# Kernel tuning notes

Hardware: AMD Instinct MI355X
Metric: run time of the kernel (lower is better)

The kernel has to match this reference:

```python
import jax, jax.numpy as jnp
import numpy as np

D_MODEL = 1024
H = 16
DH = 64
FFN = 4096
CHUNK = 64
LN_EPS = 1e-5


def layer_norm(x, w, b):
    mu = x.mean(-1, keepdims=True)
    var = x.var(-1, keepdims=True)
    return (x - mu) * jax.lax.rsqrt(var + LN_EPS) * w + b


def l2_normalize(x):
    # matches torch F.normalize(p=2, dim=-1, eps=1e-12)
    n = jnp.sqrt(jnp.sum(x * x, axis=-1, keepdims=True))
    return x / jnp.maximum(n, 1e-12)


def chunk_gla(q, k, v, alpha, C=CHUNK):
    B, Hh, N, D = q.shape
    nc = N // C  # N chosen as multiple of C (pad==0 in original)
    q = q.reshape(B, Hh, nc, C, D)
    k = k.reshape(B, Hh, nc, C, D)
    v = v.reshape(B, Hh, nc, C, D)
    alpha = alpha.reshape(B, Hh, nc, C, D)

    log_a = jnp.log(jnp.maximum(alpha, 1e-6))
    la_cum = jnp.cumsum(log_a, axis=3)                  # (B,H,nc,C,D)
    la_mean = la_cum.mean(-1)                            # (B,H,nc,C)
    tril = jnp.tril(jnp.ones((C, C), dtype=q.dtype))
    decay = jnp.exp(la_mean[..., :, None] - la_mean[..., None, :]) * tril  # (B,H,nc,C,C)

    attn_intra = jnp.einsum('bhncd,bhnmd->bhncm', q, k) * decay
    o_intra = jnp.einsum('bhncm,bhnmd->bhncd', attn_intra, v)

    decay_to_end = jnp.exp(la_cum[:, :, :, -1:, :] - la_cum)
    kv_chunk = jnp.einsum('bhncf,bhnce->bhnfe', k * decay_to_end, v)  # (B,H,nc,D,D)
    chunk_decay = jnp.exp(log_a.sum(3))                  # (B,H,nc,D)
    q_dec = q * jnp.exp(la_cum)                          # decay_from_start

    def step(S, inp):
        qd, kv, cd = inp                                 # (B,H,C,D),(B,H,D,D),(B,H,D)
        o = jnp.einsum('bhcd,bhde->bhce', qd, S)
        S_new = S * cd[:, :, :, None] + kv
        return S_new, o

    S0 = jnp.zeros((B, Hh, D, D), dtype=q.dtype)
    _, o_inter = jax.lax.scan(
        step, S0,
        (jnp.moveaxis(q_dec, 2, 0), jnp.moveaxis(kv_chunk, 2, 0), jnp.moveaxis(chunk_decay, 2, 0)))
    o_inter = jnp.moveaxis(o_inter, 0, 2)                # (B,H,nc,C,D)
    return (o_intra + o_inter).reshape(B, Hh, N, D)


def setup_inputs() -> dict:
    key = jax.random.key(0)
    ks = jax.random.split(key, 16)
    s = 0.02
    td = H * DH
    return {
        'x': jax.random.normal(ks[0], (2, 4096, D_MODEL), dtype=jnp.float32),
        'Wq': jax.random.normal(ks[1], (D_MODEL, td), dtype=jnp.float32) * s,
        'Wk': jax.random.normal(ks[2], (D_MODEL, td), dtype=jnp.float32) * s,
        'Wv': jax.random.normal(ks[3], (D_MODEL, td), dtype=jnp.float32) * s,
        'Wg': jax.random.normal(ks[4], (D_MODEL, td), dtype=jnp.float32) * s,
        'bg': jnp.full((td,), -0.5, dtype=jnp.float32),
        'Wo': jax.random.normal(ks[5], (td, D_MODEL), dtype=jnp.float32) * s,
        'ln1_w': jnp.ones((D_MODEL,), jnp.float32),
        'ln1_b': jnp.zeros((D_MODEL,), jnp.float32),
        'ln2_w': jnp.ones((D_MODEL,), jnp.float32),
        'ln2_b': jnp.zeros((D_MODEL,), jnp.float32),
        'W1': jax.random.normal(ks[6], (D_MODEL, FFN), dtype=jnp.float32) * s,
        'b1': jnp.zeros((FFN,), jnp.float32),
        'W2': jax.random.normal(ks[7], (FFN, D_MODEL), dtype=jnp.float32) * s,
        'b2': jnp.zeros((D_MODEL,), jnp.float32),
    }


def reference(x, Wq, Wk, Wv, Wg, bg, Wo, ln1_w, ln1_b, ln2_w, ln2_b, W1, b1, W2, b2):
    B, N, _ = x.shape
    xn = layer_norm(x, ln1_w, ln1_b)
    q = (xn @ Wq).reshape(B, N, H, DH).transpose(0, 2, 1, 3)
    k = (xn @ Wk).reshape(B, N, H, DH).transpose(0, 2, 1, 3)
    v = (xn @ Wv).reshape(B, N, H, DH).transpose(0, 2, 1, 3)
    q = l2_normalize(q)
    k = l2_normalize(k)
    alpha = jax.nn.sigmoid(xn @ Wg + bg).reshape(B, N, H, DH).transpose(0, 2, 1, 3)
    o = chunk_gla(q, k, v, alpha)
    o = o.transpose(0, 2, 1, 3).reshape(B, N, H * DH)
    x = x + o @ Wo  # dropout off (eval / p=0)
    h = layer_norm(x, ln2_w, ln2_b)
    x = x + jax.nn.gelu(h @ W1 + b1, approximate=False) @ W2 + b2
    return x
```

## Files before the change

kernel.cpp:

```cpp
#include <hip/hip_runtime.h>

#define AS1 __attribute__((address_space(1)))
#define AS3 __attribute__((address_space(3)))

typedef unsigned short u16;
typedef short s16x8 __attribute__((ext_vector_type(8)));
typedef float f32x4 __attribute__((ext_vector_type(4)));
typedef float f32x16 __attribute__((ext_vector_type(16)));

__device__ __forceinline__ float bf2f(u16 u) {
    union { unsigned u; float f; } v; v.u = ((unsigned)u) << 16; return v.f;
}
__device__ __forceinline__ u16 f2bf(float f) {
    union { float f; unsigned u; } v; v.f = f;
    unsigned u = v.u;
    return (u16)((u + 0x7FFFu + ((u >> 16) & 1u)) >> 16);
}

__device__ __forceinline__ void gload16(const void* g, void* l) {
    __builtin_amdgcn_global_load_lds((const AS1 void*)g, (AS3 void*)l, 16, 0, 0);
}

__global__ __launch_bounds__(256) void transpose_bf16(
    const float* __restrict__ src, u16* __restrict__ dst, int R, int C)
{
    __shared__ float t[32][33];
    const int tx = threadIdx.x, ty = threadIdx.y;
    const int r0 = blockIdx.x * 32, c0 = blockIdx.y * 32;
#pragma unroll
    for (int i = 0; i < 4; i++)
        t[ty + i * 8][tx] = src[(size_t)(r0 + ty + i * 8) * C + c0 + tx];
    __syncthreads();
#pragma unroll
    for (int i = 0; i < 4; i++)
        dst[(size_t)(c0 + ty + i * 8) * R + r0 + tx] = f2bf(t[tx][ty + i * 8]);
}

__global__ __launch_bounds__(256) void ln_bf16(
    const float* __restrict__ x, const float* __restrict__ w,
    const float* __restrict__ b, u16* __restrict__ out)
{
    __shared__ float red[8];
    const int row = blockIdx.x;
    const int tid = threadIdx.x;
    const size_t base = (size_t)row * 1024 + tid * 4;
    const float4 xv = *(const float4*)&x[base];
    float s = xv.x + xv.y + xv.z + xv.w;
    float q = xv.x * xv.x + xv.y * xv.y + xv.z * xv.z + xv.w * xv.w;
#pragma unroll
    for (int m = 1; m < 64; m <<= 1) { s += __shfl_xor(s, m); q += __shfl_xor(q, m); }
    if ((tid & 63) == 0) { red[tid >> 6] = s; red[4 + (tid >> 6)] = q; }
    __syncthreads();
    s = red[0] + red[1] + red[2] + red[3];
    q = red[4] + red[5] + red[6] + red[7];
    const float mu = s * (1.f / 1024.f);
    const float var = q * (1.f / 1024.f) - mu * mu;
    const float rs = rsqrtf(var + 1e-5f);
    const float4 wv = *(const float4*)&w[tid * 4];
    const float4 bv = *(const float4*)&b[tid * 4];
    uint2 ov;
    ov.x = (unsigned)f2bf((xv.x - mu) * rs * wv.x + bv.x) |
           ((unsigned)f2bf((xv.y - mu) * rs * wv.y + bv.y) << 16);
    ov.y = (unsigned)f2bf((xv.z - mu) * rs * wv.z + bv.z) |
           ((unsigned)f2bf((xv.w - mu) * rs * wv.w + bv.w) << 16);
    *(uint2*)&out[base] = ov;
}

template <int EPX>
__global__ __launch_bounds__(256, 3) void gemmS(
    const u16* __restrict__ A, const u16* __restrict__ BT,
    float* __restrict__ Cf, u16* __restrict__ Cb,
    const float* __restrict__ bias, const float* __restrict__ resid,
    int M, int N, int K)
{
    __shared__ u16 As[8192];
    __shared__ u16 Bs[8192];
    const int tid = threadIdx.x;
    const int w = tid >> 6, l = tid & 63;

    const int gx = gridDim.x;
    const int nb = gx * gridDim.y;
    const int bid0 = blockIdx.y * gx + blockIdx.x;
    const int swz = (bid0 & 7) * (nb >> 3) + (bid0 >> 3);
    const int tm = (swz % gx) * 128;
    const int tn = (swz / gx) * 128;

    const int wm = (w >> 1) * 64, wn = (w & 1) * 64;

    const int srow = l >> 3;
    const int sg = ((l & 7) ^ srow) * 8;
    size_t aSb[4], bSb[4];
#pragma unroll
    for (int j = 0; j < 4; j++) {
        aSb[j] = (size_t)(tm + j * 32 + w * 8 + srow) * K + sg;
        bSb[j] = (size_t)(tn + j * 32 + w * 8 + srow) * K + sg;
    }

    const int la = l & 31, hi = l >> 5, key = l & 7;
    int aoff[2][4], boff[2][4];
#pragma unroll
    for (int mm = 0; mm < 2; mm++)
#pragma unroll
        for (int ks = 0; ks < 4; ks++) {
            const int g = ((ks * 2 + hi) ^ key) * 8;
            aoff[mm][ks] = (wm + mm * 32 + la) * 64 + g;
            boff[mm][ks] = (wn + mm * 32 + la) * 64 + g;
        }

    f32x16 acc[2][2] = {};

#pragma unroll
    for (int j = 0; j < 4; j++) {
        gload16(&A[aSb[j]], &As[(j * 32 + w * 8) * 64]);
        gload16(&BT[bSb[j]], &Bs[(j * 32 + w * 8) * 64]);
    }

    const int NT = K >> 6;
    for (int t = 0; t < NT; ++t) {
        __syncthreads();
#pragma unroll
        for (int ks = 0; ks < 4; ks++) {
            s16x8 a0 = *(const s16x8*)&As[aoff[0][ks]];
            s16x8 a1 = *(const s16x8*)&As[aoff[1][ks]];
            s16x8 b0 = *(const s16x8*)&Bs[boff[0][ks]];
            s16x8 b1 = *(const s16x8*)&Bs[boff[1][ks]];
            acc[0][0] = __builtin_amdgcn_mfma_f32_32x32x16_bf16(a0, b0, acc[0][0], 0, 0, 0);
            acc[0][1] = __builtin_amdgcn_mfma_f32_32x32x16_bf16(a0, b1, acc[0][1], 0, 0, 0);
            acc[1][0] = __builtin_amdgcn_mfma_f32_32x32x16_bf16(a1, b0, acc[1][0], 0, 0, 0);
            acc[1][1] = __builtin_amdgcn_mfma_f32_32x32x16_bf16(a1, b1, acc[1][1], 0, 0, 0);
        }
        if (t + 1 < NT) {
            __syncthreads();
            const int k0 = (t + 1) * 64;
#pragma unroll
            for (int j = 0; j < 4; j++) {
                gload16(&A[aSb[j] + k0], &As[(j * 32 + w * 8) * 64]);
                gload16(&BT[bSb[j] + k0], &Bs[(j * 32 + w * 8) * 64]);
            }
        }
    }

#pragma unroll
    for (int mm = 0; mm < 2; mm++)
#pragma unroll
        for (int nn = 0; nn < 2; nn++)
#pragma unroll
            for (int reg = 0; reg < 16; reg++) {
                const int row = tm + wm + mm * 32 + hi * 4 + (reg & 3) + (reg >> 2) * 8;
                const int col = tn + wn + nn * 32 + la;
                const float v = acc[mm][nn][reg];
                if (EPX == 0) {
                    if (col < 3072) Cb[(size_t)row * 3072 + col] = f2bf(v);
                    else            Cf[(size_t)row * 1024 + (col - 3072)] = v;
                } else if (EPX == 1) {
                    const float u2 = v + bias[col];
                    Cb[(size_t)row * N + col] =
                        f2bf(0.5f * u2 * (1.f + erff(u2 * 0.70710678118654752f)));
                } else if (EPX == 2) {
                    const size_t idx = (size_t)row * N + col;
                    Cf[idx] = v + resid[idx];
                } else {
                    const size_t idx = (size_t)row * N + col;
                    Cf[idx] = v + bias[col] + resid[idx];
                }
            }
}

#define TP 72
#define LP 65
__global__ __launch_bounds__(256) void gla_a(
    const u16* __restrict__ qkv,
    const float* __restrict__ g,
    const float* __restrict__ bg,
    u16* __restrict__ qdec,
    u16* __restrict__ kvT,
    float* __restrict__ cdec,
    u16* __restrict__ ointra)
{
    __shared__ u16 Qh[64 * TP];
    __shared__ u16 Kh[64 * TP];
    __shared__ u16 VT[64 * TP];
    __shared__ float L[64 * LP];
    __shared__ float lm[64], nq[64], nk[64];

    const int bid = blockIdx.x;
    const int bh = bid >> 6, ck = bid & 63;
    const int b = bh >> 4, h = bh & 15;
    const int tok0 = b * 4096 + ck * 64;
    const int tid = threadIdx.x;
    const int w = tid >> 6, l = tid & 63;

#pragma unroll
    for (int pass = 0; pass < 2; pass++) {
        const int c = (tid >> 3) + pass * 32;
        const int col = (tid & 7) * 8;
        const size_t rb = (size_t)(tok0 + c) * 3072 + h * 64 + col;
        uint4 qv = *(const uint4*)&qkv[rb];
        uint4 kv_ = *(const uint4*)&qkv[rb + 1024];
        uint4 vv = *(const uint4*)&qkv[rb + 2048];
        *(uint4*)&Qh[c * TP + col] = qv;
        *(uint4*)&Kh[c * TP + col] = kv_;
        const u16* va = (const u16*)&vv;
#pragma unroll
        for (int j = 0; j < 8; j++) VT[(col + j) * TP + c] = va[j];
    }
#pragma unroll
    for (int pass = 0; pass < 4; pass++) {
        const int c = (tid >> 4) + pass * 16;
        const int col = (tid & 15) * 4;
        float4 gv = *(const float4*)&g[(size_t)(tok0 + c) * 1024 + h * 64 + col];
        float4 bgv = *(const float4*)&bg[h * 64 + col];
        const float* ga = (const float*)&gv;
        const float* ba = (const float*)&bgv;
#pragma unroll
        for (int i = 0; i < 4; i++) {
            const float z = ga[i] + ba[i];
            const float al = 1.f / (1.f + __expf(-z));
            L[c * LP + col + i] = __logf(fmaxf(al, 1e-6f));
        }
    }
    __syncthreads();

    {
        const int d = tid >> 2, qq = tid & 3;
        float vals[16];
#pragma unroll
        for (int i = 0; i < 16; i++) vals[i] = L[(qq * 16 + i) * LP + d];
        float s = 0.f;
#pragma unroll
        for (int i = 0; i < 16; i++) { s += vals[i]; vals[i] = s; }
        float sum = s;
        float u1 = __shfl_up(sum, 1, 4); if (qq >= 1) sum += u1;
        float u2 = __shfl_up(sum, 2, 4); if (qq >= 2) sum += u2;
        const float excl = sum - s;
#pragma unroll
        for (int i = 0; i < 16; i++) L[(qq * 16 + i) * LP + d] = vals[i] + excl;
        if (qq == 3) cdec[((size_t)bh * 64 + ck) * 64 + d] = __expf(sum);
    }
    __syncthreads();

    {
        const int c = tid >> 2, qq = tid & 3;
        float sl = 0.f, sq = 0.f, sk = 0.f;
        uint4 qa = *(const uint4*)&Qh[c * TP + qq * 16];
        uint4 qb = *(const uint4*)&Qh[c * TP + qq * 16 + 8];
        uint4 ka = *(const uint4*)&Kh[c * TP + qq * 16];
        uint4 kb = *(const uint4*)&Kh[c * TP + qq * 16 + 8];
        const u16* qu = (const u16*)&qa; const u16* qu2 = (const u16*)&qb;
        const u16* ku = (const u16*)&ka; const u16* ku2 = (const u16*)&kb;
#pragma unroll
        for (int i = 0; i < 8; i++) {
            float q1 = bf2f(qu[i]), q2 = bf2f(qu2[i]);
            float k1 = bf2f(ku[i]), k2 = bf2f(ku2[i]);
            sq += q1 * q1 + q2 * q2;
            sk += k1 * k1 + k2 * k2;
        }
#pragma unroll
        for (int i = 0; i < 16; i++) sl += L[c * LP + qq * 16 + i];
        sl += __shfl_xor(sl, 1); sl += __shfl_xor(sl, 2);
        sq += __shfl_xor(sq, 1); sq += __shfl_xor(sq, 2);
        sk += __shfl_xor(sk, 1); sk += __shfl_xor(sk, 2);
        if (qq == 0) {
            lm[c] = sl * (1.f / 64.f);
            nq[c] = 1.f / fmaxf(sqrtf(sq), 1e-12f);
            nk[c] = 1.f / fmaxf(sqrtf(sk), 1e-12f);
        }
    }
    __syncthreads();

    u16 kdt[16];
    {
        const int c = tid >> 2, qq = tid & 3;
        const float qn = nq[c], kn = nk[c];
        uint4 qa = *(const uint4*)&Qh[c * TP + qq * 16];
        uint4 qb = *(const uint4*)&Qh[c * TP + qq * 16 + 8];
        uint4 ka = *(const uint4*)&Kh[c * TP + qq * 16];
        uint4 kb = *(const uint4*)&Kh[c * TP + qq * 16 + 8];
        u16* qu = (u16*)&qa; u16* qu2 = (u16*)&qb;
        u16* ku = (u16*)&ka; u16* ku2 = (u16*)&kb;
        float Lc[16], Le[16];
#pragma unroll
        for (int i = 0; i < 16; i++) {
            Lc[i] = L[c * LP + qq * 16 + i];
            Le[i] = L[63 * LP + qq * 16 + i];
        }
        unsigned pk[8];
#pragma unroll
        for (int i = 0; i < 8; i++) {
            float qh1 = bf2f(qu[i]) * qn;  qu[i] = f2bf(qh1);
            float qh2 = bf2f(qu2[i]) * qn; qu2[i] = f2bf(qh2);
            float kh1 = bf2f(ku[i]) * kn;  ku[i] = f2bf(kh1);
            float kh2 = bf2f(ku2[i]) * kn; ku2[i] = f2bf(kh2);
            kdt[i]     = f2bf(kh1 * __expf(Le[i] - Lc[i]));
            kdt[i + 8] = f2bf(kh2 * __expf(Le[i + 8] - Lc[i + 8]));
        }
#pragma unroll
        for (int i = 0; i < 4; i++) {
            pk[i] = (unsigned)f2bf(bf2f(qu[2 * i]) * __expf(Lc[2 * i])) |
                    ((unsigned)f2bf(bf2f(qu[2 * i + 1]) * __expf(Lc[2 * i + 1])) << 16);
            pk[4 + i] = (unsigned)f2bf(bf2f(qu2[2 * i]) * __expf(Lc[8 + 2 * i])) |
                        ((unsigned)f2bf(bf2f(qu2[2 * i + 1]) * __expf(Lc[8 + 2 * i + 1])) << 16);
        }
        *(uint4*)&Qh[c * TP + qq * 16] = qa;
        *(uint4*)&Qh[c * TP + qq * 16 + 8] = qb;
        *(uint4*)&Kh[c * TP + qq * 16] = ka;
        *(uint4*)&Kh[c * TP + qq * 16 + 8] = kb;
        u16* qrow = &qdec[((size_t)bh * 4096 + ck * 64 + c) * 64 + qq * 16];
        *(uint4*)&qrow[0] = *(const uint4*)&pk[0];
        *(uint4*)&qrow[8] = *(const uint4*)&pk[4];
    }
    __syncthreads();

    u16* KDT = (u16*)L;
    {
        const int c = tid >> 2, qq = tid & 3;
#pragma unroll
        for (int i = 0; i < 16; i++) KDT[(qq * 16 + i) * TP + c] = kdt[i];
    }
    const int fr = l & 15;
    const int kk = (l >> 4) * 8;
    f32x4 accS[4] = {};
#pragma unroll
    for (int ks = 0; ks < 2; ks++) {
        s16x8 af = *(const s16x8*)&Qh[(w * 16 + fr) * TP + ks * 32 + kk];
#pragma unroll
        for (int j = 0; j < 4; j++) {
            s16x8 bf = *(const s16x8*)&Kh[(j * 16 + fr) * TP + ks * 32 + kk];
            accS[j] = __builtin_amdgcn_mfma_f32_16x16x32_bf16(af, bf, accS[j], 0, 0, 0);
        }
    }
    __syncthreads();

    {
        const int erow = w * 16 + (l >> 4) * 4;
#pragma unroll
        for (int j = 0; j < 4; j++) {
            const int mm = j * 16 + (l & 15);
            const float lmm = lm[mm];
#pragma unroll
            for (int r = 0; r < 4; r++) {
                const int cc = erow + r;
                const float wgt = (mm <= cc) ? __expf(lm[cc] - lmm) : 0.f;
                Qh[cc * TP + mm] = f2bf(accS[j][r] * wgt);
            }
        }
    }
    __syncthreads();

    f32x4 accO[4] = {};
    f32x4 accK[4] = {};
#pragma unroll
    for (int ks = 0; ks < 2; ks++) {
        s16x8 aAt = *(const s16x8*)&Qh[(w * 16 + fr) * TP + ks * 32 + kk];
        s16x8 aVt = *(const s16x8*)&VT[(w * 16 + fr) * TP + ks * 32 + kk];
#pragma unroll
        for (int j = 0; j < 4; j++) {
            s16x8 bVt = *(const s16x8*)&VT[(j * 16 + fr) * TP + ks * 32 + kk];
            s16x8 bKd = *(const s16x8*)&KDT[(j * 16 + fr) * TP + ks * 32 + kk];
            accO[j] = __builtin_amdgcn_mfma_f32_16x16x32_bf16(aAt, bVt, accO[j], 0, 0, 0);
            accK[j] = __builtin_amdgcn_mfma_f32_16x16x32_bf16(aVt, bKd, accK[j], 0, 0, 0);
        }
    }
    {
        const int erow = w * 16 + (l >> 4) * 4;
#pragma unroll
        for (int j = 0; j < 4; j++) {
            const int col = j * 16 + (l & 15);
#pragma unroll
            for (int r = 0; r < 4; r++) {
                const int row = erow + r;
                ointra[((size_t)bh * 4096 + ck * 64 + row) * 64 + col] = f2bf(accO[j][r]);
                kvT[(((size_t)bh * 64 + ck) * 64 + row) * 64 + col] = f2bf(accK[j][r]);
            }
        }
    }
}

__global__ __launch_bounds__(256) void gla_scan(
    const u16* __restrict__ kvT, const float* __restrict__ cdec,
    u16* __restrict__ ST)
{
    const int bh = blockIdx.x >> 4;
    const int de = (blockIdx.x & 15) * 256 + threadIdx.x;
    const int d = de & 63;
    float s = 0.f;
    const size_t base = (size_t)bh * 64 * 4096 + de;
    const size_t cb = (size_t)bh * 4096 + d;
    for (int t = 0; t < 64; t++) {
        ST[base + (size_t)t * 4096] = f2bf(s);
        s = s * cdec[cb + (size_t)t * 64] + bf2f(kvT[base + (size_t)t * 4096]);
    }
}

__global__ __launch_bounds__(256) void gla_b(
    const u16* __restrict__ qdec, const u16* __restrict__ ST,
    const u16* __restrict__ ointra, u16* __restrict__ obf)
{
    __shared__ u16 Qd[64 * TP];
    __shared__ u16 Sd[64 * TP];
    const int bid = blockIdx.x;
    const int bh = bid >> 6, ck = bid & 63;
    const int b = bh >> 4, h = bh & 15;
    const int tid = threadIdx.x;
    const int w = tid >> 6, l = tid & 63;
#pragma unroll
    for (int pass = 0; pass < 2; pass++) {
        const int r = (tid >> 3) + pass * 32;
        const int col = (tid & 7) * 8;
        *(uint4*)&Qd[r * TP + col] =
            *(const uint4*)&qdec[((size_t)bh * 4096 + ck * 64 + r) * 64 + col];
        *(uint4*)&Sd[r * TP + col] =
            *(const uint4*)&ST[(((size_t)bh * 64 + ck) * 64 + r) * 64 + col];
    }
    __syncthreads();
    const int fr = l & 15;
    const int kk = (l >> 4) * 8;
    f32x4 acc[4] = {};
#pragma unroll
    for (int ks = 0; ks < 2; ks++) {
        s16x8 af = *(const s16x8*)&Qd[(w * 16 + fr) * TP + ks * 32 + kk];
#pragma unroll
        for (int j = 0; j < 4; j++) {
            s16x8 bf = *(const s16x8*)&Sd[(j * 16 + fr) * TP + ks * 32 + kk];
            acc[j] = __builtin_amdgcn_mfma_f32_16x16x32_bf16(af, bf, acc[j], 0, 0, 0);
        }
    }
    const int erow = w * 16 + (l >> 4) * 4;
#pragma unroll
    for (int j = 0; j < 4; j++) {
        const int e = j * 16 + (l & 15);
#pragma unroll
        for (int r = 0; r < 4; r++) {
            const int cc = erow + r;
            const size_t ia = ((size_t)bh * 4096 + ck * 64 + cc) * 64 + e;
            const float v = acc[j][r] + bf2f(ointra[ia]);
            obf[(size_t)(b * 4096 + ck * 64 + cc) * 1024 + h * 64 + e] = f2bf(v);
        }
    }
}

__global__ void fill_sentinel(float* out, int n) {
    int i = blockIdx.x * 256 + threadIdx.x;
    if (i < n) out[i] = 12345.0f;
}

extern "C" void kernel_launch(void* const* d_in, const int* in_sizes, int n_in,
                              void* d_out, int out_size, void* d_ws, size_t ws_size,
                              hipStream_t stream)
{
    const float* x    = (const float*)d_in[0];
    const float* Wq   = (const float*)d_in[1];
    const float* Wk   = (const float*)d_in[2];
    const float* Wv   = (const float*)d_in[3];
    const float* Wg   = (const float*)d_in[4];
    const float* bg   = (const float*)d_in[5];
    const float* Wo   = (const float*)d_in[6];
    const float* ln1w = (const float*)d_in[7];
    const float* ln1b = (const float*)d_in[8];
    const float* ln2w = (const float*)d_in[9];
    const float* ln2b = (const float*)d_in[10];
    const float* W1   = (const float*)d_in[11];
    const float* b1   = (const float*)d_in[12];
    const float* W2   = (const float*)d_in[13];
    const float* b2   = (const float*)d_in[14];
    float* out = (float*)d_out;

    char* ws = (char*)d_ws;
    u16*   wtQKVG = (u16*)(ws + 0);
    u16*   wtWo   = (u16*)(ws + 8388608);
    u16*   wtW1   = (u16*)(ws + 10485760);
    u16*   wtW2   = (u16*)(ws + 18874368);
    u16*   xnb    = (u16*)(ws + 27262976);
    u16*   qkvb   = (u16*)(ws + 44040192);
    float* gbuf   = (float*)(ws + 94371840);
    u16*   kvT    = (u16*)(ws + 127926272);
    float* cdbuf  = (float*)(ws + 144703488);
    u16*   qdecb  = (u16*)(ws + 145227776);
    u16*   ointra = (u16*)(ws + 162004992);
    u16*   STb    = (u16*)(ws + 178782208);
    u16*   obf    = (u16*)(ws + 195559424);
    u16*   hbf    = (u16*)(ws + 212336640);
    float* x2     = (float*)(ws + 94371840);
    u16*   ffnb   = (u16*)(ws + 27262976);

    if (ws_size < 229113856u) {
        fill_sentinel<<<dim3((out_size + 255) / 256), dim3(256), 0, stream>>>(out, out_size);
        return;
    }

    const dim3 b256(256), b32x8(32, 8);

    transpose_bf16<<<dim3(32, 32),  b32x8, 0, stream>>>(Wq, wtQKVG,               1024, 1024);
    transpose_bf16<<<dim3(32, 32),  b32x8, 0, stream>>>(Wk, wtQKVG + 1024 * 1024, 1024, 1024);
    transpose_bf16<<<dim3(32, 32),  b32x8, 0, stream>>>(Wv, wtQKVG + 2048 * 1024, 1024, 1024);
    transpose_bf16<<<dim3(32, 32),  b32x8, 0, stream>>>(Wg, wtQKVG + 3072 * 1024, 1024, 1024);
    transpose_bf16<<<dim3(32, 32),  b32x8, 0, stream>>>(Wo, wtWo,                 1024, 1024);
    transpose_bf16<<<dim3(32, 128), b32x8, 0, stream>>>(W1, wtW1,                 1024, 4096);
    transpose_bf16<<<dim3(128, 32), b32x8, 0, stream>>>(W2, wtW2,                 4096, 1024);

    ln_bf16<<<dim3(8192), b256, 0, stream>>>(x, ln1w, ln1b, xnb);
    gemmS<0><<<dim3(64, 32), b256, 0, stream>>>(xnb, wtQKVG, gbuf, qkvb, nullptr, nullptr, 8192, 4096, 1024);

    gla_a<<<dim3(2048), b256, 0, stream>>>(qkvb, gbuf, bg, qdecb, kvT, cdbuf, ointra);
    gla_scan<<<dim3(512), b256, 0, stream>>>(kvT, cdbuf, STb);
    gla_b<<<dim3(2048), b256, 0, stream>>>(qdecb, STb, ointra, obf);

    gemmS<2><<<dim3(64, 8), b256, 0, stream>>>(obf, wtWo, x2, nullptr, nullptr, x, 8192, 1024, 1024);
    ln_bf16<<<dim3(8192), b256, 0, stream>>>(x2, ln2w, ln2b, hbf);
    gemmS<1><<<dim3(64, 32), b256, 0, stream>>>(hbf, wtW1, nullptr, ffnb, b1, nullptr, 8192, 4096, 1024);
    gemmS<4><<<dim3(64, 8), b256, 0, stream>>>(ffnb, wtW2, out, nullptr, b2, x2, 8192, 1024, 4096);
}
```

Before: 454.3 us.

## Add 256x128 tile GEMM for wide QKVG and FFN1 projections

Introduces a new gemmW kernel with a 256x128 output tile (each wave computing 128x64), used for the two N=4096 GEMMs (QKVG projection and FFN up with GELU). The goal is more reuse of the B tile per block and fewer LDS loads per MFMA. The cost is more LDS, a larger accumulator register footprint and occupancy dropping to 2 blocks. It also removes the block-index swizzle from gemmS, which may hurt L2 locality for the remaining N=1024 GEMMs.

```diff
diff --git a/kernel.cpp b/kernel.cpp
--- a/kernel.cpp
+++ b/kernel.cpp
@@ -67,9 +67,96 @@
 }
 
 template <int EPX>
+__global__ __launch_bounds__(256, 2) void gemmW(
+    const u16* __restrict__ A, const u16* __restrict__ BT,
+    float* __restrict__ Cf, u16* __restrict__ Cb,
+    const float* __restrict__ bias, int M, int N, int K)
+{
+    __shared__ u16 As[256 * 64];
+    __shared__ u16 Bs[128 * 64];
+    const int tid = threadIdx.x;
+    const int w = tid >> 6, l = tid & 63;
+    const int tm = blockIdx.x * 256, tn = blockIdx.y * 128;
+    const int wr = w >> 1, wc = w & 1;
+
+    const int srow = l >> 3;
+    const int sg = ((l & 7) ^ srow) * 8;
+    size_t aSb[8], bSb[4];
+#pragma unroll
+    for (int j = 0; j < 8; j++)
+        aSb[j] = (size_t)(tm + w * 64 + j * 8 + srow) * K + sg;
+#pragma unroll
+    for (int j = 0; j < 4; j++)
+        bSb[j] = (size_t)(tn + w * 32 + j * 8 + srow) * K + sg;
+
+    const int la = l & 31, hi = l >> 5, key = l & 7;
+    int aoff[4][4], boff[2][4];
+#pragma unroll
+    for (int mm = 0; mm < 4; mm++)
+#pragma unroll
+        for (int ks = 0; ks < 4; ks++)
+            aoff[mm][ks] = (wr * 128 + mm * 32 + la) * 64 + (((ks * 2 + hi)) ^ key) * 8;
+#pragma unroll
+    for (int nn = 0; nn < 2; nn++)
+#pragma unroll
+        for (int ks = 0; ks < 4; ks++)
+            boff[nn][ks] = (wc * 64 + nn * 32 + la) * 64 + (((ks * 2 + hi)) ^ key) * 8;
+
+    f32x16 acc[4][2] = {};
+
+#pragma unroll
+    for (int j = 0; j < 8; j++) gload16(&A[aSb[j]], &As[(w * 64 + j * 8) * 64]);
+#pragma unroll
+    for (int j = 0; j < 4; j++) gload16(&BT[bSb[j]], &Bs[(w * 32 + j * 8) * 64]);
+
+    const int NT = K >> 6;
+    for (int t = 0; t < NT; ++t) {
+        __syncthreads();
+#pragma unroll
+        for (int ks = 0; ks < 4; ks++) {
+            s16x8 b0 = *(const s16x8*)&Bs[boff[0][ks]];
+            s16x8 b1 = *(const s16x8*)&Bs[boff[1][ks]];
+#pragma unroll
+            for (int mm = 0; mm < 4; mm++) {
+                s16x8 a0 = *(const s16x8*)&As[aoff[mm][ks]];
+                acc[mm][0] = __builtin_amdgcn_mfma_f32_32x32x16_bf16(a0, b0, acc[mm][0], 0, 0, 0);
+                acc[mm][1] = __builtin_amdgcn_mfma_f32_32x32x16_bf16(a0, b1, acc[mm][1], 0, 0, 0);
+            }
+        }
+        if (t + 1 < NT) {
+            __syncthreads();
+            const int k0 = (t + 1) * 64;
+#pragma unroll
+            for (int j = 0; j < 8; j++) gload16(&A[aSb[j] + k0], &As[(w * 64 + j * 8) * 64]);
+#pragma unroll
+            for (int j = 0; j < 4; j++) gload16(&BT[bSb[j] + k0], &Bs[(w * 32 + j * 8) * 64]);
+        }
+    }
+
+#pragma unroll
+    for (int mm = 0; mm < 4; mm++)
+#pragma unroll
+        for (int nn = 0; nn < 2; nn++)
+#pragma unroll
+            for (int reg = 0; reg < 16; reg++) {
+                const int row = tm + wr * 128 + mm * 32 + hi * 4 + (reg & 3) + (reg >> 2) * 8;
+                const int col = tn + wc * 64 + nn * 32 + la;
+                const float v = acc[mm][nn][reg];
+                if (EPX == 0) {
+                    if (col < 3072) Cb[(size_t)row * 3072 + col] = f2bf(v);
+                    else            Cf[(size_t)row * 1024 + (col - 3072)] = v;
+                } else {
+                    const float u2 = v + bias[col];
+                    Cb[(size_t)row * N + col] =
+                        f2bf(0.5f * u2 * (1.f + erff(u2 * 0.70710678118654752f)));
+                }
+            }
+}
+
+template <int EPX>
 __global__ __launch_bounds__(256, 3) void gemmS(
     const u16* __restrict__ A, const u16* __restrict__ BT,
-    float* __restrict__ Cf, u16* __restrict__ Cb,
+    float* __restrict__ Cf,
     const float* __restrict__ bias, const float* __restrict__ resid,
     int M, int N, int K)
 {
@@ -77,14 +164,7 @@
     __shared__ u16 Bs[8192];
     const int tid = threadIdx.x;
     const int w = tid >> 6, l = tid & 63;
-
-    const int gx = gridDim.x;
-    const int nb = gx * gridDim.y;
-    const int bid0 = blockIdx.y * gx + blockIdx.x;
-    const int swz = (bid0 & 7) * (nb >> 3) + (bid0 >> 3);
-    const int tm = (swz % gx) * 128;
-    const int tn = (swz / gx) * 128;
-
+    const int tm = blockIdx.x * 128, tn = blockIdx.y * 128;
     const int wm = (w >> 1) * 64, wn = (w & 1) * 64;
 
     const int srow = l >> 3;
@@ -149,20 +229,9 @@
                 const int row = tm + wm + mm * 32 + hi * 4 + (reg & 3) + (reg >> 2) * 8;
                 const int col = tn + wn + nn * 32 + la;
                 const float v = acc[mm][nn][reg];
-                if (EPX == 0) {
-                    if (col < 3072) Cb[(size_t)row * 3072 + col] = f2bf(v);
-                    else            Cf[(size_t)row * 1024 + (col - 3072)] = v;
-                } else if (EPX == 1) {
-                    const float u2 = v + bias[col];
-                    Cb[(size_t)row * N + col] =
-                        f2bf(0.5f * u2 * (1.f + erff(u2 * 0.70710678118654752f)));
-                } else if (EPX == 2) {
-                    const size_t idx = (size_t)row * N + col;
-                    Cf[idx] = v + resid[idx];
-                } else {
-                    const size_t idx = (size_t)row * N + col;
-                    Cf[idx] = v + bias[col] + resid[idx];
-                }
+                const size_t idx = (size_t)row * N + col;
+                if (EPX == 2) Cf[idx] = v + resid[idx];
+                else          Cf[idx] = v + bias[col] + resid[idx];
             }
 }
 
@@ -499,14 +568,14 @@
     transpose_bf16<<<dim3(128, 32), b32x8, 0, stream>>>(W2, wtW2,                 4096, 1024);
 
     ln_bf16<<<dim3(8192), b256, 0, stream>>>(x, ln1w, ln1b, xnb);
-    gemmS<0><<<dim3(64, 32), b256, 0, stream>>>(xnb, wtQKVG, gbuf, qkvb, nullptr, nullptr, 8192, 4096, 1024);
+    gemmW<0><<<dim3(32, 32), b256, 0, stream>>>(xnb, wtQKVG, gbuf, qkvb, nullptr, 8192, 4096, 1024);
 
     gla_a<<<dim3(2048), b256, 0, stream>>>(qkvb, gbuf, bg, qdecb, kvT, cdbuf, ointra);
     gla_scan<<<dim3(512), b256, 0, stream>>>(kvT, cdbuf, STb);
     gla_b<<<dim3(2048), b256, 0, stream>>>(qdecb, STb, ointra, obf);
 
-    gemmS<2><<<dim3(64, 8), b256, 0, stream>>>(obf, wtWo, x2, nullptr, nullptr, x, 8192, 1024, 1024);
+    gemmS<2><<<dim3(64, 8), b256, 0, stream>>>(obf, wtWo, x2, nullptr, x, 8192, 1024, 1024);
     ln_bf16<<<dim3(8192), b256, 0, stream>>>(x2, ln2w, ln2b, hbf);
-    gemmS<1><<<dim3(64, 32), b256, 0, stream>>>(hbf, wtW1, nullptr, ffnb, b1, nullptr, 8192, 4096, 1024);
-    gemmS<4><<<dim3(64, 8), b256, 0, stream>>>(ffnb, wtW2, out, nullptr, b2, x2, 8192, 1024, 4096);
-}
+    gemmW<1><<<dim3(32, 32), b256, 0, stream>>>(hbf, wtW1, nullptr, ffnb, b1, 8192, 4096, 1024);
+    gemmS<4><<<dim3(64, 8), b256, 0, stream>>>(ffnb, wtW2, out, b2, x2, 8192, 1024, 4096);
+}
```

After: 545.7 us. +20.1%, slower.
